# Optimization experiments

Hardware: AMD Instinct MI355X
Metric: run time of the kernel (lower is better)

## Reference

```python
import jax, jax.numpy as jnp
import numpy as np

HIDDEN = 1024
NUM_HEADS = 16
HEAD_SIZE = HIDDEN // NUM_HEADS


def setup_inputs() -> dict:
    key = jax.random.key(0)
    ks = jax.random.split(key, 5)
    B, S = 2, 2048
    x = jax.random.normal(ks[0], (B, S, HIDDEN), dtype=jnp.float32)
    # nn.Linear(hidden, 3*hidden): weight stored (in, out) for x @ W
    scale_qkv = 1.0 / np.sqrt(HIDDEN)
    w_qkv = jax.random.uniform(ks[1], (HIDDEN, 3 * HIDDEN), minval=-scale_qkv, maxval=scale_qkv, dtype=jnp.float32)
    b_qkv = jax.random.uniform(ks[2], (3 * HIDDEN,), minval=-scale_qkv, maxval=scale_qkv, dtype=jnp.float32)
    w_o = jax.random.uniform(ks[3], (HIDDEN, HIDDEN), minval=-scale_qkv, maxval=scale_qkv, dtype=jnp.float32)
    b_o = jax.random.uniform(ks[4], (HIDDEN,), minval=-scale_qkv, maxval=scale_qkv, dtype=jnp.float32)
    return {"x": x, "w_qkv": w_qkv, "b_qkv": b_qkv, "w_o": w_o, "b_o": b_o}


def reference(x, w_qkv, b_qkv, w_o, b_o):
    B, S, H = x.shape
    qkv = x @ w_qkv + b_qkv  # (B, S, 3H)
    q, k, v = jnp.split(qkv, 3, axis=-1)
    # (B, S, H) -> (B, nheads, S, head_size)
    def heads(t):
        return t.reshape(B, S, NUM_HEADS, HEAD_SIZE).transpose(0, 2, 1, 3)
    q, k, v = heads(q), heads(k), heads(v)
    scores = jnp.einsum('bhqd,bhkd->bhqk', q, k) / np.sqrt(HEAD_SIZE).astype(np.float32)
    causal = jnp.tril(jnp.ones((S, S), dtype=bool))  # k <= q
    scores = jnp.where(causal, scores, -jnp.inf)
    probs = jax.nn.softmax(scores, axis=-1)
    out = jnp.einsum('bhqk,bhkd->bqhd', probs, v).reshape(B, S, H)
    return out @ w_o + b_o
```

## Files before the change

kernel.cpp:

```cpp
#include <hip/hip_runtime.h>
#include <stdint.h>


typedef __bf16 bf16;
typedef __attribute__((ext_vector_type(8))) __bf16 bf16x8;
typedef __attribute__((ext_vector_type(4))) __bf16 bf16x4;
typedef __attribute__((ext_vector_type(4))) float floatx4;

#define SCL 0.18033688011112042f

__device__ __forceinline__ floatx4 mfma_bf16(bf16x8 a, bf16x8 b, floatx4 c) {
  return __builtin_amdgcn_mfma_f32_16x16x32_bf16(a, b, c, 0, 0, 0);
}

__device__ __forceinline__ void cp_g2l_16(const bf16* g, bf16* l) {
  __builtin_amdgcn_global_load_lds(
      (const __attribute__((address_space(1))) void*)g,
      (__attribute__((address_space(3))) void*)l, 16, 0, 0);
}

__global__ __launch_bounds__(256) void prep_kernel(
    const float* __restrict__ x, bf16* __restrict__ xb,
    const float* __restrict__ w_qkv, bf16* __restrict__ wqkvt,
    const float* __restrict__ w_o, bf16* __restrict__ wot) {
  const int b = blockIdx.x;
  const int tid = threadIdx.x;
  if (b < 4096) {
    const int i = (b * 256 + tid) * 4;
    floatx4 v = *(const floatx4*)(x + i);
    bf16x4 o;
    o[0] = (bf16)v[0]; o[1] = (bf16)v[1]; o[2] = (bf16)v[2]; o[3] = (bf16)v[3];
    *(bf16x4*)(xb + i) = o;
    return;
  }
  __shared__ float tile[32][33];
  const float* W; bf16* Wt; int K, N, n0, k0;
  if (b < 7168) {
    const int bb = b - 4096;
    W = w_qkv; Wt = wqkvt; K = 1024; N = 3072;
    n0 = (bb % 96) * 32; k0 = (bb / 96) * 32;
  } else {
    const int bb = b - 7168;
    W = w_o; Wt = wot; K = 1024; N = 1024;
    n0 = (bb & 31) * 32; k0 = (bb >> 5) * 32;
  }
  const int tx = tid & 31, ty = tid >> 5;
  for (int i = 0; i < 4; ++i)
    tile[ty + 8 * i][tx] = W[(size_t)(k0 + ty + 8 * i) * N + n0 + tx];
  __syncthreads();
  for (int i = 0; i < 4; ++i)
    Wt[(size_t)(n0 + ty + 8 * i) * K + k0 + tx] = (bf16)tile[tx][ty + 8 * i];
}

template <int MODE, int MI>
__global__ __launch_bounds__(256, 3) void gemm_bt_kernel(
    const bf16* __restrict__ A, const bf16* __restrict__ Bt,
    const float* __restrict__ bias, float* __restrict__ outF,
    bf16* __restrict__ qb, bf16* __restrict__ kb, bf16* __restrict__ vtb,
    int N, int K) {
  constexpr int BM = MI * 32;
  __shared__ bf16 As[BM * 32];
  __shared__ bf16 Bs[128 * 32];
  const int tid = threadIdx.x;
  const int w = tid >> 6, lane = tid & 63;
  const int l16 = lane & 15, quad = lane >> 4;
  const int m0 = blockIdx.y * BM, n0 = blockIdx.x * 128;
  const int wm = (w & 1) * (BM / 2), wn = (w >> 1) * 64;

  const int arow = w * (BM / 4) + (lane >> 2);
  const int acol = (lane & 3) * 8;
  const bf16* Ag = A + (size_t)(m0 + arow) * K + acol;
  bf16* Al = As + arow * 32 + acol;
  const int brow = w * 32 + (lane >> 2);
  const bf16* Bg = Bt + (size_t)(n0 + brow) * K + acol;
  bf16* Bl = Bs + brow * 32 + acol;

  floatx4 acc[MI][4];
#pragma unroll
  for (int i = 0; i < MI; ++i)
#pragma unroll
    for (int j = 0; j < 4; ++j) acc[i][j] = (floatx4){0.f, 0.f, 0.f, 0.f};

  for (int k0 = 0; k0 < K; k0 += 32) {
    __syncthreads();
    cp_g2l_16(Ag + k0, Al);
    if (MI == 4) cp_g2l_16(Ag + (size_t)16 * K + k0, Al + 16 * 32);
    cp_g2l_16(Bg + k0, Bl);
    cp_g2l_16(Bg + (size_t)16 * K + k0, Bl + 16 * 32);
    __syncthreads();
    bf16x8 af[MI], bfr[4];
#pragma unroll
    for (int i = 0; i < MI; ++i)
      af[i] = *(const bf16x8*)(&As[(wm + i * 16 + l16) * 32 + quad * 8]);
#pragma unroll
    for (int j = 0; j < 4; ++j)
      bfr[j] = *(const bf16x8*)(&Bs[(wn + j * 16 + l16) * 32 + quad * 8]);
#pragma unroll
    for (int i = 0; i < MI; ++i)
#pragma unroll
      for (int j = 0; j < 4; ++j)
        acc[i][j] = mfma_bf16(af[i], bfr[j], acc[i][j]);
  }

#pragma unroll
  for (int i = 0; i < MI; ++i)
#pragma unroll
    for (int j = 0; j < 4; ++j) {
      const int nn = n0 + wn + j * 16 + l16;
      const float bv = bias[nn];
      const int mbase = m0 + wm + i * 16 + quad * 4;
      if (MODE == 1) {
#pragma unroll
        for (int r = 0; r < 4; ++r)
          outF[(size_t)(mbase + r) * N + nn] = acc[i][j][r] + bv;
      } else {
        const int which = nn >> 10;
        const int rem = nn & 1023;
        const int h = rem >> 6, d = rem & 63;
        const int b = mbase >> 11, s = mbase & 2047;
        const size_t bh = (size_t)(b * 16 + h);
        if (which == 2) {
          bf16x4 pk;
#pragma unroll
          for (int r = 0; r < 4; ++r) pk[r] = (bf16)(acc[i][j][r] + bv);
          *(bf16x4*)(vtb + (bh * 64 + d) * 2048 + s) = pk;
        } else if (which == 0) {
#pragma unroll
          for (int r = 0; r < 4; ++r)
            qb[(bh * 2048 + s + r) * 64 + d] = (bf16)((acc[i][j][r] + bv) * SCL);
        } else {
#pragma unroll
          for (int r = 0; r < 4; ++r)
            kb[(bh * 2048 + s + r) * 64 + d] = (bf16)(acc[i][j][r] + bv);
        }
      }
    }
}

__global__ __launch_bounds__(256, 3) void attn_kernel(
    const bf16* __restrict__ Qb, const bf16* __restrict__ Kb,
    const bf16* __restrict__ Vtb, bf16* __restrict__ attnb) {
  __shared__ bf16 Ks[4096];
  __shared__ bf16 Vs[4096];
  __shared__ bf16 Ps[4 * 2368];
  const int bid = blockIdx.x;
  const int bh = (bid & 7) * 4 + ((bid >> 3) & 3);
  const int qblk = 15 - (bid >> 5);
  const int tid = threadIdx.x;
  const int w = tid >> 6, lane = tid & 63;
  const int l16 = lane & 15, quad = lane >> 4;
  const int q0 = qblk * 128 + w * 32;
  const int b = bh >> 4, h = bh & 15;
  const bf16* Qh = Qb + (size_t)bh * 2048 * 64;
  const bf16* Kh = Kb + (size_t)bh * 2048 * 64;
  const bf16* Vh = Vtb + (size_t)bh * 64 * 2048;
  bf16* Pw = Ps + w * 2368;
  const int pw_wr = quad * 288 + (quad >> 1) * 16 + l16;
  const int pw_rd = l16 * 72 + (l16 >> 3) * 16 + quad * 8;

  const int nt = 2 * qblk + 2;
  const int wdiag = q0 >> 6;

  const int c0 = tid, c1 = 256 + tid;
  const int ksrc0 = (c0 >> 3) * 64 + (((c0 & 7) - (c0 >> 3)) & 7) * 8;
  const int ksrc1 = (c1 >> 3) * 64 + (((c1 & 7) - (c1 >> 3)) & 7) * 8;
  const int vsrc0 = (c0 >> 3) * 2048 + (((c0 & 7) - (c0 >> 3)) & 7) * 8;
  const int vsrc1 = (c1 >> 3) * 2048 + (((c1 & 7) - (c1 >> 3)) & 7) * 8;
  bf16* kdst0 = Ks + c0 * 8; bf16* kdst1 = Ks + c1 * 8;
  bf16* vdst0 = Vs + c0 * 8; bf16* vdst1 = Vs + c1 * 8;

  bf16x8 qf[2][2];
#pragma unroll
  for (int mb = 0; mb < 2; ++mb)
#pragma unroll
    for (int kq = 0; kq < 2; ++kq)
      qf[mb][kq] = *(const bf16x8*)(Qh + (size_t)(q0 + mb * 16 + l16) * 64 +
                                    kq * 32 + quad * 8);
  bf16x8 ones;
#pragma unroll
  for (int j = 0; j < 8; ++j) ones[j] = (bf16)1.0f;

  floatx4 O[2][4], Ol[2];
#pragma unroll
  for (int mb = 0; mb < 2; ++mb) {
#pragma unroll
    for (int nd = 0; nd < 4; ++nd) O[mb][nd] = (floatx4){0.f, 0.f, 0.f, 0.f};
    Ol[mb] = (floatx4){0.f, 0.f, 0.f, 0.f};
  }

  for (int t = 0; t < nt; ++t) {
    __syncthreads();
    {
      const bf16* KtG = Kh + (size_t)t * 4096;
      const bf16* VtG = Vh + t * 64;
      cp_g2l_16(KtG + ksrc0, kdst0);
      cp_g2l_16(KtG + ksrc1, kdst1);
      cp_g2l_16(VtG + vsrc0, vdst0);
      cp_g2l_16(VtG + vsrc1, vdst1);
    }
    __syncthreads();

    if (t > wdiag) continue;
    const bool diag = (t == wdiag);

    bf16x8 kf[4][2];
#pragma unroll
    for (int nk = 0; nk < 4; ++nk)
#pragma unroll
      for (int kq = 0; kq < 2; ++kq) {
        const int row = nk * 16 + l16;
        kf[nk][kq] = *(const bf16x8*)(
            &Ks[row * 64 + ((kq * 4 + quad + row) & 7) * 8]);
      }

    {
      floatx4 sf[4];
#pragma unroll
      for (int nk = 0; nk < 4; ++nk) {
        floatx4 a = (floatx4){0.f, 0.f, 0.f, 0.f};
        a = mfma_bf16(qf[0][0], kf[nk][0], a);
        a = mfma_bf16(qf[0][1], kf[nk][1], a);
        sf[nk] = a;
      }
#pragma unroll
      for (int nk = 0; nk < 4; ++nk)
#pragma unroll
        for (int r = 0; r < 4; ++r) {
          float s = sf[nk][r];
          if (diag) {
            const int kc = t * 64 + nk * 16 + l16;
            const int qrow = q0 + quad * 4 + r;
            s = (kc <= qrow) ? s : -1e30f;
          }
          Pw[pw_wr + r * 72 + nk * 16] = (bf16)__builtin_amdgcn_exp2f(s);
        }
    }
    floatx4 sg[4];
#pragma unroll
    for (int nk = 0; nk < 4; ++nk) {
      floatx4 a = (floatx4){0.f, 0.f, 0.f, 0.f};
      a = mfma_bf16(qf[1][0], kf[nk][0], a);
      a = mfma_bf16(qf[1][1], kf[nk][1], a);
      sg[nk] = a;
    }
    bf16x8 vf[4][2];
#pragma unroll
    for (int nd = 0; nd < 4; ++nd)
#pragma unroll
      for (int kq = 0; kq < 2; ++kq) {
        const int row = nd * 16 + l16;
        vf[nd][kq] = *(const bf16x8*)(
            &Vs[row * 64 + ((kq * 4 + quad + row) & 7) * 8]);
      }
#pragma unroll
    for (int nk = 0; nk < 4; ++nk)
#pragma unroll
      for (int r = 0; r < 4; ++r) {
        float s = sg[nk][r];
        if (diag) {
          const int kc = t * 64 + nk * 16 + l16;
          const int qrow = q0 + 16 + quad * 4 + r;
          s = (kc <= qrow) ? s : -1e30f;
        }
        Pw[pw_wr + 1184 + r * 72 + nk * 16] = (bf16)__builtin_amdgcn_exp2f(s);
      }

#pragma unroll
    for (int mb = 0; mb < 2; ++mb) {
      bf16x8 pf[2];
      pf[0] = *(const bf16x8*)(&Pw[pw_rd + mb * 1184]);
      pf[1] = *(const bf16x8*)(&Pw[pw_rd + mb * 1184 + 32]);
#pragma unroll
      for (int nd = 0; nd < 4; ++nd) {
        floatx4 o = O[mb][nd];
        o = mfma_bf16(pf[0], vf[nd][0], o);
        o = mfma_bf16(pf[1], vf[nd][1], o);
        O[mb][nd] = o;
      }
      Ol[mb] = mfma_bf16(pf[0], ones, Ol[mb]);
      Ol[mb] = mfma_bf16(pf[1], ones, Ol[mb]);
    }
  }

#pragma unroll
  for (int mb = 0; mb < 2; ++mb)
#pragma unroll
    for (int r = 0; r < 4; ++r) {
      const int qrow = q0 + mb * 16 + quad * 4 + r;
      const float inv = 1.f / Ol[mb][r];
#pragma unroll
      for (int nd = 0; nd < 4; ++nd)
        attnb[((size_t)(b * 2048 + qrow)) * 1024 + h * 64 + nd * 16 + l16] =
            (bf16)(O[mb][nd][r] * inv);
    }
}

extern "C" void kernel_launch(void* const* d_in, const int* in_sizes, int n_in,
                              void* d_out, int out_size, void* d_ws, size_t ws_size,
                              hipStream_t stream) {
  const float* x     = (const float*)d_in[0];
  const float* w_qkv = (const float*)d_in[1];
  const float* b_qkv = (const float*)d_in[2];
  const float* w_o   = (const float*)d_in[3];
  const float* b_o   = (const float*)d_in[4];
  float* out = (float*)d_out;

  char* ws = (char*)d_ws;
  bf16* xb    = (bf16*)ws; ws += (size_t)4096 * 1024 * 2;
  bf16* wqkvt = (bf16*)ws; ws += (size_t)3072 * 1024 * 2;
  bf16* wot   = (bf16*)ws; ws += (size_t)1024 * 1024 * 2;
  bf16* qb    = (bf16*)ws; ws += (size_t)32 * 2048 * 64 * 2;
  bf16* kb    = (bf16*)ws; ws += (size_t)32 * 2048 * 64 * 2;
  bf16* vtb   = (bf16*)ws; ws += (size_t)32 * 2048 * 64 * 2;
  bf16* attnb = (bf16*)ws; ws += (size_t)4096 * 1024 * 2;

  prep_kernel<<<8192, 256, 0, stream>>>(x, xb, w_qkv, wqkvt, w_o, wot);
  gemm_bt_kernel<0, 4><<<dim3(24, 32), 256, 0, stream>>>(
      xb, wqkvt, b_qkv, nullptr, qb, kb, vtb, 3072, 1024);
  attn_kernel<<<512, 256, 0, stream>>>(qb, kb, vtb, attnb);
  gemm_bt_kernel<1, 2><<<dim3(8, 64), 256, 0, stream>>>(
      attnb, wot, b_o, out, nullptr, nullptr, nullptr, 1024, 1024);
}
```

Before: 189.1 us.

## Double-buffer K/V tiles in attention and pair mirrored query tiles per block

K and V tiles are now double-buffered in shared memory. The next tile's global-to-LDS load is issued right after a single barrier, so it overlaps with compute on the current tile, and the second barrier per iteration is dropped. Work is also reassigned: each block's first two waves handle query tile p and the other two handle tile 31-p, which balances causal work across blocks. The cost is twice the K/V shared memory, which may press on 3-blocks-per-CU occupancy. Waves on the short tile also idle through the remaining iterations while still joining every barrier.

```diff
diff --git a/kernel.cpp b/kernel.cpp
--- a/kernel.cpp
+++ b/kernel.cpp
@@ -140,16 +140,17 @@
 __global__ __launch_bounds__(256, 3) void attn_kernel(
     const bf16* __restrict__ Qb, const bf16* __restrict__ Kb,
     const bf16* __restrict__ Vtb, bf16* __restrict__ attnb) {
-  __shared__ bf16 Ks[4096];
-  __shared__ bf16 Vs[4096];
+  __shared__ bf16 Ks[2][4096];
+  __shared__ bf16 Vs[2][4096];
   __shared__ bf16 Ps[4 * 2368];
   const int bid = blockIdx.x;
   const int bh = (bid & 7) * 4 + ((bid >> 3) & 3);
-  const int qblk = 15 - (bid >> 5);
+  const int p = bid >> 5;
   const int tid = threadIdx.x;
   const int w = tid >> 6, lane = tid & 63;
   const int l16 = lane & 15, quad = lane >> 4;
-  const int q0 = qblk * 128 + w * 32;
+  const int qt = (w < 2) ? p : (31 - p);
+  const int q0 = qt * 64 + (w & 1) * 32;
   const int b = bh >> 4, h = bh & 15;
   const bf16* Qh = Qb + (size_t)bh * 2048 * 64;
   const bf16* Kh = Kb + (size_t)bh * 2048 * 64;
@@ -158,16 +159,14 @@
   const int pw_wr = quad * 288 + (quad >> 1) * 16 + l16;
   const int pw_rd = l16 * 72 + (l16 >> 3) * 16 + quad * 8;
 
-  const int nt = 2 * qblk + 2;
-  const int wdiag = q0 >> 6;
+  const int nt = 32 - p;
+  const int wdiag = qt;
 
   const int c0 = tid, c1 = 256 + tid;
   const int ksrc0 = (c0 >> 3) * 64 + (((c0 & 7) - (c0 >> 3)) & 7) * 8;
   const int ksrc1 = (c1 >> 3) * 64 + (((c1 & 7) - (c1 >> 3)) & 7) * 8;
   const int vsrc0 = (c0 >> 3) * 2048 + (((c0 & 7) - (c0 >> 3)) & 7) * 8;
   const int vsrc1 = (c1 >> 3) * 2048 + (((c1 & 7) - (c1 >> 3)) & 7) * 8;
-  bf16* kdst0 = Ks + c0 * 8; bf16* kdst1 = Ks + c1 * 8;
-  bf16* vdst0 = Vs + c0 * 8; bf16* vdst1 = Vs + c1 * 8;
 
   bf16x8 qf[2][2];
 #pragma unroll
@@ -188,20 +187,28 @@
     Ol[mb] = (floatx4){0.f, 0.f, 0.f, 0.f};
   }
 
-  for (int t = 0; t < nt; ++t) {
+  cp_g2l_16(Kh + ksrc0, &Ks[0][c0 * 8]);
+  cp_g2l_16(Kh + ksrc1, &Ks[0][c1 * 8]);
+  cp_g2l_16(Vh + vsrc0, &Vs[0][c0 * 8]);
+  cp_g2l_16(Vh + vsrc1, &Vs[0][c1 * 8]);
+
+  int cur = 0;
+  for (int t = 0; t < nt; ++t, cur ^= 1) {
     __syncthreads();
-    {
-      const bf16* KtG = Kh + (size_t)t * 4096;
-      const bf16* VtG = Vh + t * 64;
-      cp_g2l_16(KtG + ksrc0, kdst0);
-      cp_g2l_16(KtG + ksrc1, kdst1);
-      cp_g2l_16(VtG + vsrc0, vdst0);
-      cp_g2l_16(VtG + vsrc1, vdst1);
-    }
-    __syncthreads();
+    if (t + 1 < nt) {
+      const bf16* KtG = Kh + (size_t)(t + 1) * 4096;
+      const bf16* VtG = Vh + (t + 1) * 64;
+      const int nb = cur ^ 1;
+      cp_g2l_16(KtG + ksrc0, &Ks[nb][c0 * 8]);
+      cp_g2l_16(KtG + ksrc1, &Ks[nb][c1 * 8]);
+      cp_g2l_16(VtG + vsrc0, &Vs[nb][c0 * 8]);
+      cp_g2l_16(VtG + vsrc1, &Vs[nb][c1 * 8]);
+    }
 
     if (t > wdiag) continue;
     const bool diag = (t == wdiag);
+    const bf16* KsC = Ks[cur];
+    const bf16* VsC = Vs[cur];
 
     bf16x8 kf[4][2];
 #pragma unroll
@@ -210,7 +217,7 @@
       for (int kq = 0; kq < 2; ++kq) {
         const int row = nk * 16 + l16;
         kf[nk][kq] = *(const bf16x8*)(
-            &Ks[row * 64 + ((kq * 4 + quad + row) & 7) * 8]);
+            &KsC[row * 64 + ((kq * 4 + quad + row) & 7) * 8]);
       }
 
     {
@@ -250,7 +257,7 @@
       for (int kq = 0; kq < 2; ++kq) {
         const int row = nd * 16 + l16;
         vf[nd][kq] = *(const bf16x8*)(
-            &Vs[row * 64 + ((kq * 4 + quad + row) & 7) * 8]);
+            &VsC[row * 64 + ((kq * 4 + quad + row) & 7) * 8]);
       }
 #pragma unroll
     for (int nk = 0; nk < 4; ++nk)
```

New measurement: 191.4 us. Within noise of the previous version (+1.2%).
